# Performance work log

Hardware: AMD Instinct MI355X
Metric: run time of the kernel (lower is better)

The kernel has to match this reference:

```python
import jax, jax.numpy as jnp
import numpy as np

HEADS = 20
HEAD_DIM = 64  # 1280 // 20
NUM_STYLE_TOKENS = 4
FU_SCALE = 0.5
STYLE_SCALE = 1.0
SCALE = np.float32(1.0 / np.sqrt(HEAD_DIM))


def setup_inputs() -> dict:
    key = jax.random.key(0)
    ks = jax.random.split(key, 9)
    B, S, D_MODEL, D_CROSS, T = 4, 4096, 1280, 768, 77
    sd_m = np.float32(1.0 / np.sqrt(D_MODEL))
    sd_c = np.float32(1.0 / np.sqrt(D_CROSS))
    return {
        "hidden_states": jax.random.normal(ks[0], (B, S, D_MODEL), jnp.float32),
        "encoder_hidden_states": jax.random.normal(ks[1], (B, T + NUM_STYLE_TOKENS, D_CROSS), jnp.float32),
        "Wq": jax.random.normal(ks[2], (D_MODEL, D_MODEL), jnp.float32) * sd_m,
        "Wk": jax.random.normal(ks[3], (D_CROSS, D_MODEL), jnp.float32) * sd_c,
        "Wv": jax.random.normal(ks[4], (D_CROSS, D_MODEL), jnp.float32) * sd_c,
        "Wk_ip": jax.random.normal(ks[5], (D_CROSS, D_MODEL), jnp.float32) * sd_c,
        "Wv_ip": jax.random.normal(ks[6], (D_CROSS, D_MODEL), jnp.float32) * sd_c,
        "Wo": jax.random.normal(ks[7], (D_MODEL, D_MODEL), jnp.float32) * sd_m,
        "bo": jnp.zeros((D_MODEL,), jnp.float32),
    }


def _split_heads(x, B):
    # [B, L, H*D] -> [B, H, L, D]
    return x.reshape(B, -1, HEADS, HEAD_DIM).transpose(0, 2, 1, 3)


def _attn_blend(q, k, v):
    # Manual QK^T softmax with cross-batch prob blending (fuAttn / fuIPAttn).
    probs = jax.nn.softmax(jnp.einsum('bhsd,bhtd->bhst', q, k) * SCALE, axis=-1)
    probs = probs.at[1].set(FU_SCALE * probs[1] + (1.0 - FU_SCALE) * probs[0])
    probs = probs.at[3].set(FU_SCALE * probs[3] + (1.0 - FU_SCALE) * probs[2])
    return jnp.einsum('bhst,bhtd->bhsd', probs, v)


def reference(hidden_states, encoder_hidden_states, Wq, Wk, Wv, Wk_ip, Wv_ip, Wo, bo):
    B, S, _ = hidden_states.shape
    end_pos = encoder_hidden_states.shape[1] - NUM_STYLE_TOKENS
    text = encoder_hidden_states[:, :end_pos, :]       # [B, 77, Dc]
    ip_style = encoder_hidden_states[:, end_pos:, :]   # [B, 4, Dc]

    q = _split_heads(hidden_states @ Wq, B)   # [B,H,S,D]
    k = _split_heads(text @ Wk, B)            # [B,H,77,D]
    v = _split_heads(text @ Wv, B)

    hid = _attn_blend(q, k, v).transpose(0, 2, 1, 3).reshape(B, S, -1)
    raw = hid

    ip_k = _split_heads(ip_style @ Wk_ip, B)  # [B,H,4,D]
    ip_v = _split_heads(ip_style @ Wv_ip, B)
    ip_hid = _attn_blend(q, ip_k, ip_v).transpose(0, 2, 1, 3).reshape(B, S, -1)

    hid = hid + STYLE_SCALE * ip_hid
    # batch rows 0 and 2 keep the raw (text-only) attention output
    hid = hid.at[0].set(raw[0]).at[2].set(raw[2])

    return hid @ Wo + bo
```

## Files before the change

kernel.cpp:

```cpp
#include <hip/hip_runtime.h>
#include <hip/hip_bf16.h>

typedef _Float16 half8 __attribute__((ext_vector_type(8)));
typedef _Float16 half4 __attribute__((ext_vector_type(4)));
typedef float floatx4 __attribute__((ext_vector_type(4)));

#define HEADS_ 20
#define B_    4
#define S_    4096
#define DM    1280
#define DC    768
#define TTOK  77
#define NST   4
#define EROWS 81
#define MROWS 324
#define NT_K  20

__device__ inline void gload_lds16(const void* g, void* l) {
  __builtin_amdgcn_global_load_lds((const __attribute__((address_space(1))) void*)g,
                                   (__attribute__((address_space(3))) void*)l, 16, 0, 0);
}

__global__ __launch_bounds__(256) void cast_f16(const float* __restrict__ in,
                                                _Float16* __restrict__ out, long n) {
  long i = ((long)blockIdx.x * 256 + threadIdx.x) * 8L;
  long stride = (long)gridDim.x * 256 * 8;
  for (; i < n; i += stride) {
    float4 a = *(const float4*)(in + i);
    float4 b = *(const float4*)(in + i + 4);
    half8 h;
    h[0] = (_Float16)a.x; h[1] = (_Float16)a.y; h[2] = (_Float16)a.z; h[3] = (_Float16)a.w;
    h[4] = (_Float16)b.x; h[5] = (_Float16)b.y; h[6] = (_Float16)b.z; h[7] = (_Float16)b.w;
    *(half8*)(out + i) = h;
  }
}

__global__ __launch_bounds__(256) void transpose_cast(const float* __restrict__ in,
                                                      _Float16* __restrict__ out,
                                                      int R, int C) {
  __shared__ float t[32][33];
  int tx = threadIdx.x & 31, ty = threadIdx.x >> 5;
  int c0 = blockIdx.x * 32, r0 = blockIdx.y * 32;
  #pragma unroll
  for (int j = 0; j < 32; j += 8)
    t[ty + j][tx] = in[(size_t)(r0 + ty + j) * C + c0 + tx];
  __syncthreads();
  #pragma unroll
  for (int j = 0; j < 32; j += 8)
    out[(size_t)(c0 + ty + j) * R + r0 + tx] = (_Float16)t[tx][ty + j];
}

struct Ptrs4 { const _Float16* B[4]; _Float16* C[4]; };

__global__ __launch_bounds__(256) void gemm_kv(const _Float16* __restrict__ A,
                                               Ptrs4 p4, int M, int K, int N) {
  const int tid = threadIdx.x, lane = tid & 63, w = tid >> 6;
  const _Float16* Bp = p4.B[blockIdx.z];
  _Float16* Ch = p4.C[blockIdx.z];
  const int bm = blockIdx.x, bn = blockIdx.y;

  __shared__ _Float16 As[128 * 32];
  __shared__ _Float16 Bs[128 * 32];

  const int wr = (w >> 1) * 64, wc = (w & 1) * 64;
  const int arow = wr + (lane & 15), brow = wc + (lane & 15);
  const int koff = (lane >> 4) * 8;
  floatx4 acc[4][4] = {};

  const int nk = K >> 5;
  for (int kt = 0; kt < nk; ++kt) {
    #pragma unroll
    for (int c = 0; c < 2; ++c) {
      int l16 = w * 64 + lane + c * 256;
      int row = l16 >> 2, kc = (l16 & 3) << 3;
      int gr = bm * 128 + row; if (gr > M - 1) gr = M - 1;
      gload_lds16(A + (size_t)gr * K + kt * 32 + kc, &As[(w + c * 4) * 512]);
      int grb = bn * 128 + row;
      gload_lds16(Bp + (size_t)grb * K + kt * 32 + kc, &Bs[(w + c * 4) * 512]);
    }
    __syncthreads();
    half8 af[4], bf[4];
    #pragma unroll
    for (int m = 0; m < 4; m++) af[m] = *(const half8*)&As[(arow + m * 16) * 32 + koff];
    #pragma unroll
    for (int n = 0; n < 4; n++) bf[n] = *(const half8*)&Bs[(brow + n * 16) * 32 + koff];
    #pragma unroll
    for (int m = 0; m < 4; m++)
      #pragma unroll
      for (int n = 0; n < 4; n++)
        acc[m][n] = __builtin_amdgcn_mfma_f32_16x16x32_f16(af[m], bf[n], acc[m][n], 0, 0, 0);
    __syncthreads();
  }

  const int r0 = (lane >> 4) * 4, c0 = lane & 15;
  #pragma unroll
  for (int m = 0; m < 4; m++) {
    #pragma unroll
    for (int r = 0; r < 4; r++) {
      int grow = bm * 128 + wr + m * 16 + r0 + r;
      if (grow >= M) continue;
      size_t base = (size_t)grow * N + bn * 128 + wc + c0;
      #pragma unroll
      for (int n = 0; n < 4; n++) Ch[base + n * 16] = (_Float16)acc[m][n][r];
    }
  }
}

template<int OMODE>
__global__ __launch_bounds__(512, 2)
void gemm8(const _Float16* __restrict__ A,
           const _Float16* __restrict__ B,
           void* __restrict__ Cout,
           const float* __restrict__ bias) {
  __shared__ _Float16 lds[57344];
  _Float16* const A0 = lds;
  _Float16* const A1 = lds + 8192;
  _Float16* const B0 = lds + 16384;
  _Float16* const B1 = lds + 36864;

  const int tid = threadIdx.x, lane = tid & 63, w = tid >> 6;
  const int swz = (blockIdx.x & 7) * 64 + (blockIdx.x >> 3);
  const int bm = swz & 127, bn = swz >> 7;

  const int wr = w >> 2, wc = w & 3;
  const int ql = lane & 15, lg = lane >> 4, xr = ql & 7;
  const int Abase = (wr * 64 + ql) * 64;
  const int Bbase = (wc * 80 + ql) * 64;

  const int srow = tid >> 3, sslot = tid & 7;
  const int scol = ((sslot ^ (srow & 7)) << 3);
  const _Float16* const Asrc = A + (size_t)(bm * 128 + srow) * DM + scol;
  const _Float16* const Bsrc = B + (size_t)(bn * 320 + srow) * DM + scol;
  const int ldst = w * 512;

  auto stage = [&](const _Float16* src, _Float16* buf, int q, int kt) {
    gload_lds16(src + (size_t)q * 64 * DM + kt * 64, buf + q * 4096 + ldst);
  };
  auto rdA = [&](const _Float16* buf, int m, int ks) -> half8 {
    return *(const half8*)(buf + Abase + m * 1024 + (((ks * 4 + lg) ^ xr) << 3));
  };
  auto rdB = [&](const _Float16* buf, int n, int ks) -> half8 {
    return *(const half8*)(buf + Bbase + n * 1024 + (((ks * 4 + lg) ^ xr) << 3));
  };

  floatx4 acc[4][5] = {};
  half8 bF[5];

  #pragma unroll
  for (int q = 0; q < 2; ++q) stage(Asrc, A0, q, 0);
  #pragma unroll
  for (int q = 0; q < 5; ++q) stage(Bsrc, B0, q, 0);

  auto tile_body = [&](const _Float16* Ac, const _Float16* Bc,
                       _Float16* An, _Float16* Bn, int j, bool pref) {
    if (pref) {
      stage(Asrc, An, 0, j + 1); stage(Bsrc, Bn, 0, j + 1);
      asm volatile("s_waitcnt vmcnt(2)" ::: "memory");
    } else {
      asm volatile("s_waitcnt vmcnt(0)" ::: "memory");
    }
    asm volatile("s_waitcnt lgkmcnt(0)" ::: "memory");
    __builtin_amdgcn_sched_barrier(0);
    __builtin_amdgcn_s_barrier();
    __builtin_amdgcn_sched_barrier(0);

    #pragma unroll
    for (int ks = 0; ks < 2; ++ks) {
      #pragma unroll
      for (int n = 0; n < 5; ++n) bF[n] = rdB(Bc, n, ks);
      if (pref) {
        if (ks == 0) { stage(Asrc, An, 1, j + 1); stage(Bsrc, Bn, 1, j + 1); }
        else         { stage(Bsrc, Bn, 3, j + 1); }
      }
      #pragma unroll
      for (int m = 0; m < 4; ++m) {
        if (m == 2 && pref) {
          if (ks == 0) { stage(Bsrc, Bn, 2, j + 1); }
          else         { stage(Bsrc, Bn, 4, j + 1); }
        }
        half8 a = rdA(Ac, m, ks);
        __builtin_amdgcn_s_setprio(1);
        #pragma unroll
        for (int n = 0; n < 5; ++n)
          acc[m][n] = __builtin_amdgcn_mfma_f32_16x16x32_f16(a, bF[n], acc[m][n], 0, 0, 0);
        __builtin_amdgcn_s_setprio(0);
      }
    }
  };

  for (int j = 0; j < NT_K; j += 2) {
    tile_body(A0, B0, A1, B1, j, true);
    tile_body(A1, B1, A0, B0, j + 1, j + 2 < NT_K);
  }

  const int r0 = lg * 4;
  if (OMODE == 1) {
    _Float16* Ch = (_Float16*)Cout;
    #pragma unroll
    for (int m = 0; m < 4; ++m)
      #pragma unroll
      for (int r = 0; r < 4; ++r) {
        size_t base = (size_t)(bm * 128 + wr * 64 + m * 16 + r0 + r) * DM + bn * 320 + wc * 80 + ql;
        #pragma unroll
        for (int n = 0; n < 5; ++n)
          Ch[base + n * 16] = (_Float16)(acc[m][n][r] * 0.125f);
      }
  } else {
    float* Cf = (float*)Cout;
    float bv[5];
    #pragma unroll
    for (int n = 0; n < 5; ++n) bv[n] = bias[bn * 320 + wc * 80 + n * 16 + ql];
    #pragma unroll
    for (int m = 0; m < 4; ++m)
      #pragma unroll
      for (int r = 0; r < 4; ++r) {
        size_t base = (size_t)(bm * 128 + wr * 64 + m * 16 + r0 + r) * DM + bn * 320 + wc * 80 + ql;
        #pragma unroll
        for (int n = 0; n < 5; ++n)
          Cf[base + n * 16] = acc[m][n][r] + bv[n];
      }
  }
}

__global__ __launch_bounds__(256) void attn_kernel(const _Float16* __restrict__ Q,
                                                   const _Float16* __restrict__ kf,
                                                   const _Float16* __restrict__ vf,
                                                   const _Float16* __restrict__ ipk,
                                                   const _Float16* __restrict__ ipv,
                                                   _Float16* __restrict__ hid) {
  const int tid = threadIdx.x;
  const int h = blockIdx.y, b = blockIdx.z;
  const bool odd = (b & 1);
  const int hoff = h * 64;
  const int lane = tid & 63, w = tid >> 6;
  const int g = lane >> 4, ql = lane & 15;

  __shared__ _Float16 K1s[96 * 64];
  __shared__ _Float16 K2s[96 * 64];
  __shared__ _Float16 VTs[64 * 104];
  __shared__ char Pl[4][16 * 208];
  char* const K1c = (char*)K1s;
  char* const K2c = (char*)K2s;
  char* const VTc = (char*)VTs;
  char* const Pwc = Pl[w];

  const half8 zero8 = {};
  for (int i = tid; i < 96 * 8; i += 256) {
    int key = i >> 3, hb = i & 7;
    int dst = (key * 128 + hb * 16) ^ ((key & 7) << 4);
    half8 v = zero8;
    if (key < TTOK)
      v = *(const half8*)(kf + (size_t)(b * EROWS + key) * DM + hoff + hb * 8);
    else if (odd && key >= 80 && key < 84)
      v = *(const half8*)(ipk + (size_t)(b * EROWS + key - 3) * DM + hoff + hb * 8);
    *(half8*)(K1c + dst) = v;
    if (odd) {
      half8 v2 = zero8;
      if (key < TTOK)
        v2 = *(const half8*)(kf + (size_t)((b - 1) * EROWS + key) * DM + hoff + hb * 8);
      else if (key >= 80 && key < 84)
        v2 = *(const half8*)(ipk + (size_t)((b - 1) * EROWS + key - 3) * DM + hoff + hb * 8);
      *(half8*)(K2c + dst) = v2;
    }
  }
  for (int i = tid; i < 96 * 64; i += 256) {
    int key = i % 96, d = i / 96;
    _Float16 v = (_Float16)0.f;
    if (key < TTOK) v = vf[(size_t)(b * EROWS + key) * DM + hoff + d];
    else if (odd && key >= 80 && key < 84)
      v = ipv[(size_t)(b * EROWS + key - 3) * DM + hoff + d];
    VTs[d * 104 + key] = v;
  }
  __syncthreads();

  for (int t = 0; t < 4; ++t) {
    const int tq0 = blockIdx.x * 256 + t * 64 + w * 16;

    const _Float16* qp = Q + (size_t)(b * S_ + tq0 + ql) * DM + hoff + g * 8;
    half8 bq0 = *(const half8*)(qp);
    half8 bq1 = *(const half8*)(qp + 32);
    half8 bq20 = zero8, bq21 = zero8;
    if (odd) {
      const _Float16* qp2 = Q + (size_t)((b - 1) * S_ + tq0 + ql) * DM + hoff + g * 8;
      bq20 = *(const half8*)(qp2);
      bq21 = *(const half8*)(qp2 + 32);
    }

    floatx4 sA[6], sB[6];
    #pragma unroll
    for (int f = 0; f < 6; ++f) {
      int key = f * 16 + ql;
      int sw = (key & 7) << 4;
      half8 a0 = *(const half8*)(K1c + ((key * 128 + g * 16) ^ sw));
      half8 a1 = *(const half8*)(K1c + ((key * 128 + g * 16 + 64) ^ sw));
      floatx4 z = {};
      sA[f] = __builtin_amdgcn_mfma_f32_16x16x32_f16(a0, bq0, z, 0, 0, 0);
      sA[f] = __builtin_amdgcn_mfma_f32_16x16x32_f16(a1, bq1, sA[f], 0, 0, 0);
    }
    if (odd) {
      #pragma unroll
      for (int f = 0; f < 6; ++f) {
        int key = f * 16 + ql;
        int sw = (key & 7) << 4;
        half8 a0 = *(const half8*)(K2c + ((key * 128 + g * 16) ^ sw));
        half8 a1 = *(const half8*)(K2c + ((key * 128 + g * 16 + 64) ^ sw));
        floatx4 z = {};
        sB[f] = __builtin_amdgcn_mfma_f32_16x16x32_f16(a0, bq20, z, 0, 0, 0);
        sB[f] = __builtin_amdgcn_mfma_f32_16x16x32_f16(a1, bq21, sB[f], 0, 0, 0);
      }
    }

    const int kb = g * 4;
    float mA = -1e30f;
    #pragma unroll
    for (int f = 0; f < 4; ++f)
      #pragma unroll
      for (int r = 0; r < 4; ++r) mA = fmaxf(mA, sA[f][r]);
    #pragma unroll
    for (int r = 0; r < 4; ++r) if (kb + r <= 12) mA = fmaxf(mA, sA[4][r]);
    mA = fmaxf(mA, __shfl_xor(mA, 16));
    mA = fmaxf(mA, __shfl_xor(mA, 32));
    float lA = 0.f;
    #pragma unroll
    for (int f = 0; f < 4; ++f)
      #pragma unroll
      for (int r = 0; r < 4; ++r) { float e = __expf(sA[f][r] - mA); sA[f][r] = e; lA += e; }
    #pragma unroll
    for (int r = 0; r < 4; ++r) {
      float e = (kb + r <= 12) ? __expf(sA[4][r] - mA) : 0.f;
      sA[4][r] = e; lA += e;
    }
    lA += __shfl_xor(lA, 16);
    lA += __shfl_xor(lA, 32);

    float mB = -1e30f, lB = 0.f, invB = 0.f, invIpA = 0.f, invIpB = 0.f;
    if (odd) {
      #pragma unroll
      for (int f = 0; f < 4; ++f)
        #pragma unroll
        for (int r = 0; r < 4; ++r) mB = fmaxf(mB, sB[f][r]);
      #pragma unroll
      for (int r = 0; r < 4; ++r) if (kb + r <= 12) mB = fmaxf(mB, sB[4][r]);
      mB = fmaxf(mB, __shfl_xor(mB, 16));
      mB = fmaxf(mB, __shfl_xor(mB, 32));
      #pragma unroll
      for (int f = 0; f < 4; ++f)
        #pragma unroll
        for (int r = 0; r < 4; ++r) { float e = __expf(sB[f][r] - mB); sB[f][r] = e; lB += e; }
      #pragma unroll
      for (int r = 0; r < 4; ++r) {
        float e = (kb + r <= 12) ? __expf(sB[4][r] - mB) : 0.f;
        sB[4][r] = e; lB += e;
      }
      lB += __shfl_xor(lB, 16);
      lB += __shfl_xor(lB, 32);
      invB = 0.5f / lB;

      float mia = fmaxf(fmaxf(sA[5][0], sA[5][1]), fmaxf(sA[5][2], sA[5][3]));
      float mib = fmaxf(fmaxf(sB[5][0], sB[5][1]), fmaxf(sB[5][2], sB[5][3]));
      float lia = 0.f, lib = 0.f;
      #pragma unroll
      for (int r = 0; r < 4; ++r) {
        float ea = __expf(sA[5][r] - mia); sA[5][r] = ea; lia += ea;
        float eb = __expf(sB[5][r] - mib); sB[5][r] = eb; lib += eb;
      }
      invIpA = 0.5f / lia;
      invIpB = 0.5f / lib;
    }
    const float invA = (odd ? 0.5f : 1.0f) / lA;

    asm volatile("s_waitcnt lgkmcnt(0)" ::: "memory");
    __builtin_amdgcn_sched_barrier(0);
    #pragma unroll
    for (int f = 0; f < 6; ++f) {
      #pragma unroll
      for (int r = 0; r < 4; ++r) {
        int key = f * 16 + g * 4 + r;
        float p;
        if (f < 5) p = odd ? (sA[f][r] * invA + sB[f][r] * invB) : (sA[f][r] * invA);
        else p = (odd && g == 0) ? (sA[5][r] * invIpA + sB[5][r] * invIpB) : 0.f;
        *(_Float16*)(Pwc + ql * 208 + key * 2) = (_Float16)p;
      }
    }
    asm volatile("s_waitcnt lgkmcnt(0)" ::: "memory");
    __builtin_amdgcn_sched_barrier(0);

    half8 pf[3];
    #pragma unroll
    for (int kf2 = 0; kf2 < 3; ++kf2)
      pf[kf2] = *(const half8*)(Pwc + ql * 208 + g * 16 + kf2 * 64);
    floatx4 acc_o[4] = {};
    #pragma unroll
    for (int dt = 0; dt < 4; ++dt)
      #pragma unroll
      for (int kf2 = 0; kf2 < 3; ++kf2) {
        half8 vfr = *(const half8*)(VTc + (dt * 16 + ql) * 208 + g * 16 + kf2 * 64);
        acc_o[dt] = __builtin_amdgcn_mfma_f32_16x16x32_f16(vfr, pf[kf2], acc_o[dt], 0, 0, 0);
      }

    #pragma unroll
    for (int dt = 0; dt < 4; ++dt) {
      half4 hv;
      #pragma unroll
      for (int r = 0; r < 4; ++r) hv[r] = (_Float16)acc_o[dt][r];
      *(half4*)(Pwc + ql * 144 + (dt * 16 + g * 4) * 2) = hv;
    }
    asm volatile("s_waitcnt lgkmcnt(0)" ::: "memory");
    __builtin_amdgcn_sched_barrier(0);
    #pragma unroll
    for (int j2 = 0; j2 < 2; ++j2) {
      int qlo = (lane >> 3) + j2 * 8, seg = lane & 7;
      half8 ov = *(const half8*)(Pwc + qlo * 144 + seg * 16);
      *(half8*)(hid + (size_t)(b * S_ + tq0 + qlo) * DM + hoff + seg * 8) = ov;
    }
    asm volatile("s_waitcnt lgkmcnt(0)" ::: "memory");
    __builtin_amdgcn_sched_barrier(0);
  }
}

extern "C" void kernel_launch(void* const* d_in, const int* in_sizes, int n_in,
                              void* d_out, int out_size, void* d_ws, size_t ws_size,
                              hipStream_t stream) {
  const float* hs   = (const float*)d_in[0];
  const float* ehs  = (const float*)d_in[1];
  const float* Wq   = (const float*)d_in[2];
  const float* Wk   = (const float*)d_in[3];
  const float* Wv   = (const float*)d_in[4];
  const float* Wkip = (const float*)d_in[5];
  const float* Wvip = (const float*)d_in[6];
  const float* Wo   = (const float*)d_in[7];
  const float* bo   = (const float*)d_in[8];
  float* out = (float*)d_out;

  char* ws = (char*)d_ws;
  size_t off = 0;
  auto alloc = [&](size_t bytes) {
    void* p = ws + off;
    off += (bytes + 255) & ~(size_t)255;
    return p;
  };
  _Float16* hs16   = (_Float16*)alloc(20971520UL * 2);
  _Float16* ehs16  = (_Float16*)alloc(248832UL * 2);
  _Float16* WqT    = (_Float16*)alloc(1638400UL * 2);
  _Float16* WoT    = (_Float16*)alloc(1638400UL * 2);
  _Float16* WkT    = (_Float16*)alloc(983040UL * 2);
  _Float16* WvT    = (_Float16*)alloc(983040UL * 2);
  _Float16* WkipT  = (_Float16*)alloc(983040UL * 2);
  _Float16* WvipT  = (_Float16*)alloc(983040UL * 2);
  _Float16* Q16    = (_Float16*)alloc(20971520UL * 2);
  _Float16* kf16   = (_Float16*)alloc(324UL * 1280 * 2);
  _Float16* vf16   = (_Float16*)alloc(324UL * 1280 * 2);
  _Float16* ipkf16 = (_Float16*)alloc(324UL * 1280 * 2);
  _Float16* ipvf16 = (_Float16*)alloc(324UL * 1280 * 2);
  _Float16* hid16 = hs16;

  cast_f16<<<2048, 256, 0, stream>>>(hs, hs16, 20971520L);
  cast_f16<<<128, 256, 0, stream>>>(ehs, ehs16, 248832L);
  transpose_cast<<<dim3(40, 40), 256, 0, stream>>>(Wq, WqT, 1280, 1280);
  transpose_cast<<<dim3(40, 40), 256, 0, stream>>>(Wo, WoT, 1280, 1280);
  transpose_cast<<<dim3(40, 24), 256, 0, stream>>>(Wk, WkT, 768, 1280);
  transpose_cast<<<dim3(40, 24), 256, 0, stream>>>(Wv, WvT, 768, 1280);
  transpose_cast<<<dim3(40, 24), 256, 0, stream>>>(Wkip, WkipT, 768, 1280);
  transpose_cast<<<dim3(40, 24), 256, 0, stream>>>(Wvip, WvipT, 768, 1280);

  Ptrs4 p4;
  p4.B[0] = WkT; p4.B[1] = WvT; p4.B[2] = WkipT; p4.B[3] = WvipT;
  p4.C[0] = kf16; p4.C[1] = vf16; p4.C[2] = ipkf16; p4.C[3] = ipvf16;

  gemm_kv<<<dim3(3, 10, 4), 256, 0, stream>>>(ehs16, p4, MROWS, DC, DM);
  gemm8<1><<<512, 512, 0, stream>>>(hs16, WqT, (void*)Q16, nullptr);
  attn_kernel<<<dim3(16, 20, 4), 256, 0, stream>>>(Q16, kf16, vf16, ipkf16, ipvf16, hid16);
  gemm8<2><<<512, 512, 0, stream>>>(hid16, WoT, (void*)out, bo);
}
```

Before: 238.9 us.

## Batch weight transposes, specialize attention by batch parity, store outputs directly

Merges the six weight transpose-cast launches into a single 3D-grid launch indexed by blockIdx.z. Splits the attention kernel into even and odd template instances, so even batches skip the second key buffer, its LDS, and the sixth QK tile (keys 80-95 are padding when there are only 77 text tokens). The output epilogue now writes half4 values straight to global memory instead of staging through LDS for coalesced half8 stores. The intent is to cut launch overhead, LDS use and wasted MFMA work, at the cost of less coalesced global writes and an extra attention launch.

```diff
diff --git a/kernel.cpp b/kernel.cpp
--- a/kernel.cpp
+++ b/kernel.cpp
@@ -35,15 +35,20 @@
   }
 }
 
-__global__ __launch_bounds__(256) void transpose_cast(const float* __restrict__ in,
-                                                      _Float16* __restrict__ out,
-                                                      int R, int C) {
+struct TParams { const float* in[6]; _Float16* out[6]; int R[6]; };
+
+__global__ __launch_bounds__(256) void transpose_cast6(TParams p) {
+  const int z = blockIdx.z;
+  const int R = p.R[z];
+  const int r0 = blockIdx.y * 32, c0 = blockIdx.x * 32;
+  if (r0 >= R) return;
+  const float* __restrict__ in = p.in[z];
+  _Float16* __restrict__ out = p.out[z];
   __shared__ float t[32][33];
   int tx = threadIdx.x & 31, ty = threadIdx.x >> 5;
-  int c0 = blockIdx.x * 32, r0 = blockIdx.y * 32;
   #pragma unroll
   for (int j = 0; j < 32; j += 8)
-    t[ty + j][tx] = in[(size_t)(r0 + ty + j) * C + c0 + tx];
+    t[ty + j][tx] = in[(size_t)(r0 + ty + j) * DM + c0 + tx];
   __syncthreads();
   #pragma unroll
   for (int j = 0; j < 32; j += 8)
@@ -222,6 +227,7 @@
   }
 }
 
+template<bool ODD>
 __global__ __launch_bounds__(256) void attn_kernel(const _Float16* __restrict__ Q,
                                                    const _Float16* __restrict__ kf,
                                                    const _Float16* __restrict__ vf,
@@ -229,14 +235,15 @@
                                                    const _Float16* __restrict__ ipv,
                                                    _Float16* __restrict__ hid) {
   const int tid = threadIdx.x;
-  const int h = blockIdx.y, b = blockIdx.z;
-  const bool odd = (b & 1);
+  const int h = blockIdx.y;
+  const int b = blockIdx.z * 2 + (ODD ? 1 : 0);
+  constexpr bool odd = ODD;
   const int hoff = h * 64;
   const int lane = tid & 63, w = tid >> 6;
   const int g = lane >> 4, ql = lane & 15;
 
   __shared__ _Float16 K1s[96 * 64];
-  __shared__ _Float16 K2s[96 * 64];
+  __shared__ _Float16 K2s[ODD ? 96 * 64 : 8];
   __shared__ _Float16 VTs[64 * 104];
   __shared__ char Pl[4][16 * 208];
   char* const K1c = (char*)K1s;
@@ -288,7 +295,7 @@
 
     floatx4 sA[6], sB[6];
     #pragma unroll
-    for (int f = 0; f < 6; ++f) {
+    for (int f = 0; f < (ODD ? 6 : 5); ++f) {
       int key = f * 16 + ql;
       int sw = (key & 7) << 4;
       half8 a0 = *(const half8*)(K1c + ((key * 128 + g * 16) ^ sw));
@@ -398,23 +405,14 @@
         acc_o[dt] = __builtin_amdgcn_mfma_f32_16x16x32_f16(vfr, pf[kf2], acc_o[dt], 0, 0, 0);
       }
 
+    _Float16* hr = hid + (size_t)(b * S_ + tq0 + ql) * DM + hoff;
     #pragma unroll
     for (int dt = 0; dt < 4; ++dt) {
       half4 hv;
       #pragma unroll
       for (int r = 0; r < 4; ++r) hv[r] = (_Float16)acc_o[dt][r];
-      *(half4*)(Pwc + ql * 144 + (dt * 16 + g * 4) * 2) = hv;
-    }
-    asm volatile("s_waitcnt lgkmcnt(0)" ::: "memory");
-    __builtin_amdgcn_sched_barrier(0);
-    #pragma unroll
-    for (int j2 = 0; j2 < 2; ++j2) {
-      int qlo = (lane >> 3) + j2 * 8, seg = lane & 7;
-      half8 ov = *(const half8*)(Pwc + qlo * 144 + seg * 16);
-      *(half8*)(hid + (size_t)(b * S_ + tq0 + qlo) * DM + hoff + seg * 8) = ov;
-    }
-    asm volatile("s_waitcnt lgkmcnt(0)" ::: "memory");
-    __builtin_amdgcn_sched_barrier(0);
+      *(half4*)(hr + dt * 16 + g * 4) = hv;
+    }
   }
 }
 
@@ -456,12 +454,15 @@
 
   cast_f16<<<2048, 256, 0, stream>>>(hs, hs16, 20971520L);
   cast_f16<<<128, 256, 0, stream>>>(ehs, ehs16, 248832L);
-  transpose_cast<<<dim3(40, 40), 256, 0, stream>>>(Wq, WqT, 1280, 1280);
-  transpose_cast<<<dim3(40, 40), 256, 0, stream>>>(Wo, WoT, 1280, 1280);
-  transpose_cast<<<dim3(40, 24), 256, 0, stream>>>(Wk, WkT, 768, 1280);
-  transpose_cast<<<dim3(40, 24), 256, 0, stream>>>(Wv, WvT, 768, 1280);
-  transpose_cast<<<dim3(40, 24), 256, 0, stream>>>(Wkip, WkipT, 768, 1280);
-  transpose_cast<<<dim3(40, 24), 256, 0, stream>>>(Wvip, WvipT, 768, 1280);
+
+  TParams tp;
+  tp.in[0] = Wq;   tp.out[0] = WqT;   tp.R[0] = 1280;
+  tp.in[1] = Wo;   tp.out[1] = WoT;   tp.R[1] = 1280;
+  tp.in[2] = Wk;   tp.out[2] = WkT;   tp.R[2] = 768;
+  tp.in[3] = Wv;   tp.out[3] = WvT;   tp.R[3] = 768;
+  tp.in[4] = Wkip; tp.out[4] = WkipT; tp.R[4] = 768;
+  tp.in[5] = Wvip; tp.out[5] = WvipT; tp.R[5] = 768;
+  transpose_cast6<<<dim3(40, 40, 6), 256, 0, stream>>>(tp);
 
   Ptrs4 p4;
   p4.B[0] = WkT; p4.B[1] = WvT; p4.B[2] = WkipT; p4.B[3] = WvipT;
@@ -469,6 +470,7 @@
 
   gemm_kv<<<dim3(3, 10, 4), 256, 0, stream>>>(ehs16, p4, MROWS, DC, DM);
   gemm8<1><<<512, 512, 0, stream>>>(hs16, WqT, (void*)Q16, nullptr);
-  attn_kernel<<<dim3(16, 20, 4), 256, 0, stream>>>(Q16, kf16, vf16, ipkf16, ipvf16, hid16);
+  attn_kernel<false><<<dim3(16, 20, 2), 256, 0, stream>>>(Q16, kf16, vf16, ipkf16, ipvf16, hid16);
+  attn_kernel<true><<<dim3(16, 20, 2), 256, 0, stream>>>(Q16, kf16, vf16, ipkf16, ipvf16, hid16);
   gemm8<2><<<512, 512, 0, stream>>>(hid16, WoT, (void*)out, bo);
 }
```

Result: faster. 233.2 us (-2.4%).
